# Performance work log

Hardware: AMD Instinct MI355X
Metric: run time of the kernel (lower is better)

Reference implementation:

```python
import jax, jax.numpy as jnp
import numpy as np

# Sampled 2-layer GraphSAGE sizes (ogbn-products-like, fanouts [25, 10], batch 4096)
N0, N1, N2 = 1_000_000, 40_960, 4_096   # source nodes per hop / targets
E1, E2 = 1_024_000, 40_960              # edges per hop
IN_C, HID, OUT = 100, 256, 47


def setup_inputs() -> dict:
    key = jax.random.key(0)
    ks = jax.random.split(key, 10)
    x = jax.random.normal(ks[0], (N0, IN_C), jnp.float32)
    src1 = jax.random.randint(ks[1], (E1,), 0, N0, dtype=jnp.int64)
    dst1 = jax.random.randint(ks[2], (E1,), 0, N1, dtype=jnp.int64)
    src2 = jax.random.randint(ks[3], (E2,), 0, N1, dtype=jnp.int64)
    dst2 = jax.random.randint(ks[4], (E2,), 0, N2, dtype=jnp.int64)
    s1 = 1.0 / np.sqrt(IN_C)
    s2 = 1.0 / np.sqrt(HID)
    W1l = jax.random.uniform(ks[5], (IN_C, HID), jnp.float32, -s1, s1)
    W1r = jax.random.uniform(ks[6], (IN_C, HID), jnp.float32, -s1, s1)
    b1l = jnp.zeros((HID,), jnp.float32)
    W2l = jax.random.uniform(ks[7], (HID, OUT), jnp.float32, -s2, s2)
    W2r = jax.random.uniform(ks[8], (HID, OUT), jnp.float32, -s2, s2)
    b2l = jnp.zeros((OUT,), jnp.float32)
    return {"x": x, "W1l": W1l, "b1l": b1l, "W1r": W1r,
            "W2l": W2l, "b2l": b2l, "W2r": W2r,
            "src1": src1, "dst1": dst1, "src2": src2, "dst2": dst2}


def _sage_conv(x_src, x_dst, src, dst, Wl, bl, Wr, num_dst):
    # PyG SAGEConv (aggr='mean'): lin_l(mean_j x_j) + lin_r(x_target)
    msg = x_src[src]                                            # [E, C] gather
    agg = jax.ops.segment_sum(msg, dst, num_segments=num_dst)   # [num_dst, C]
    cnt = jax.ops.segment_sum(jnp.ones((src.shape[0], 1), x_src.dtype), dst,
                              num_segments=num_dst)
    agg = agg / jnp.maximum(cnt, 1.0)                           # mean (0 for isolated)
    return agg @ Wl + bl + x_dst @ Wr


def reference(x, W1l, b1l, W1r, W2l, b2l, W2r, src1, dst1, src2, dst2):
    # layer 1: bipartite (N0 -> N1)
    h = _sage_conv(x, x[:N1], src1, dst1, W1l, b1l, W1r, N1)
    h = jax.nn.relu(h)  # dropout is identity in eval mode
    # layer 2: bipartite (N1 -> N2)
    out = _sage_conv(h, h[:N2], src2, dst2, W2l, b2l, W2r, N2)
    return jax.nn.log_softmax(out, axis=-1)
```

## Files before the change

kernel.cpp:

```cpp
#include <hip/hip_runtime.h>
#include <math.h>

#define N0 1000000
#define N1 40960
#define N2 4096
#define E1 1024000
#define E2 40960
#define IN_C 100
#define HID 256
#define OUT_C 47
#define S1 128
#define S2 64
#define KCAT 224
#define KSTEPS 7
#define LDSTR 232

typedef __attribute__((ext_vector_type(8))) short short8;
typedef __attribute__((ext_vector_type(4))) float float4v;

__device__ inline unsigned short f2bf(float f) {
    union { float f; unsigned u; } v; v.f = f;
    unsigned r = v.u + 0x7FFF + ((v.u >> 16) & 1);
    return (unsigned short)(r >> 16);
}

#define EDGE_BLKS ((E1 / 2 + E2 / 2) / 256)
#define PACK_BLKS 28
__global__ __launch_bounds__(256) void build_kernel(
    const int* __restrict__ src1, const int* __restrict__ dst1,
    const int* __restrict__ src2, const int* __restrict__ dst2,
    int* __restrict__ deg1, int* __restrict__ ell1,
    int* __restrict__ deg2, int* __restrict__ ell2,
    const float* __restrict__ W1l, const float* __restrict__ W1r,
    unsigned short* __restrict__ packedW) {
    if (blockIdx.x >= EDGE_BLKS) {
        int t = (blockIdx.x - EDGE_BLKS) * 256 + threadIdx.x;
        int nt = t / 448;
        int rem = t - nt * 448;
        int ks = rem >> 6;
        int lane = rem & 63;
        int n = nt * 16 + (lane & 15);
        int kbase = ks * 32 + (lane >> 4) * 8;
        unsigned short* wp = packedW + (size_t)(nt * 7 + ks) * 512 + lane * 8;
        #pragma unroll
        for (int j = 0; j < 8; ++j) {
            int k = kbase + j;
            float v = (k < 100) ? W1l[k * HID + n]
                    : (k < 200) ? W1r[(k - 100) * HID + n] : 0.f;
            wp[j] = f2bf(v);
        }
        return;
    }
    int gid = blockIdx.x * 256 + threadIdx.x;
    if (gid < E1 / 2) {
        int2 s = ((const int2*)src1)[gid];
        int2 d = ((const int2*)dst1)[gid];
        int slot0 = atomicAdd(&deg1[d.x], 1);
        if (slot0 < S1) ell1[d.x * S1 + slot0] = s.x;
        int slot1 = atomicAdd(&deg1[d.y], 1);
        if (slot1 < S1) ell1[d.y * S1 + slot1] = s.y;
    } else {
        int p = gid - E1 / 2;
        int2 s = ((const int2*)src2)[p];
        int2 d = ((const int2*)dst2)[p];
        int slot0 = atomicAdd(&deg2[d.x], 1);
        if (slot0 < S2) ell2[d.x * S2 + slot0] = s.x;
        int slot1 = atomicAdd(&deg2[d.y], 1);
        if (slot1 < S2) ell2[d.y * S2 + slot1] = s.y;
    }
}

__global__ __launch_bounds__(256) void agg_gemm1_kernel(
    const float* __restrict__ x, const int* __restrict__ ell1,
    const int* __restrict__ deg1,
    const unsigned short* __restrict__ packedW, const float* __restrict__ b1l,
    float* __restrict__ h) {
    __shared__ short As[32 * LDSTR];
    int tid = threadIdx.x;
    int i0 = blockIdx.x * 32;
    int lane = tid & 63;
    int w = tid >> 6;

    const float2* xs2 = (const float2*)(x + (size_t)i0 * IN_C);
    for (int idx = tid; idx < 32 * 50; idx += 256) {
        int r = idx / 50;
        int p = idx - r * 50;
        float2 v = xs2[idx];
        short2 o = {(short)f2bf(v.x), (short)f2bf(v.y)};
        *(short2*)(As + r * LDSTR + 100 + 2 * p) = o;
    }
    for (int idx = tid; idx < 32 * 12; idx += 256) {
        int r = idx / 12;
        int p = idx - r * 12;
        short2 z = {0, 0};
        *(short2*)(As + r * LDSTR + 200 + 2 * p) = z;
    }

    int l2 = (lane < 50) ? lane : 49;
    for (int rr = 0; rr < 8; ++rr) {
        int d = i0 + w * 8 + rr;
        int nd = deg1[d];
        int n = (nd < S1) ? nd : S1;
        const int* rp = ell1 + d * S1;

        float x0 = 0.f, y0 = 0.f, x1 = 0.f, y1 = 0.f;
        float x2 = 0.f, y2 = 0.f, x3 = 0.f, y3 = 0.f;
        int e = 0;
        for (; e + 7 < n; e += 8) {
            int s0 = rp[e],     s1 = rp[e + 1], s2 = rp[e + 2], s3 = rp[e + 3];
            int s4 = rp[e + 4], s5 = rp[e + 5], s6 = rp[e + 6], s7 = rp[e + 7];
            float2 v0 = ((const float2*)(x + s0 * IN_C))[l2];
            float2 v1 = ((const float2*)(x + s1 * IN_C))[l2];
            float2 v2 = ((const float2*)(x + s2 * IN_C))[l2];
            float2 v3 = ((const float2*)(x + s3 * IN_C))[l2];
            float2 v4 = ((const float2*)(x + s4 * IN_C))[l2];
            float2 v5 = ((const float2*)(x + s5 * IN_C))[l2];
            float2 v6 = ((const float2*)(x + s6 * IN_C))[l2];
            float2 v7 = ((const float2*)(x + s7 * IN_C))[l2];
            x0 += v0.x + v4.x; y0 += v0.y + v4.y;
            x1 += v1.x + v5.x; y1 += v1.y + v5.y;
            x2 += v2.x + v6.x; y2 += v2.y + v6.y;
            x3 += v3.x + v7.x; y3 += v3.y + v7.y;
        }
        for (; e + 1 < n; e += 2) {
            int s0 = rp[e], s1 = rp[e + 1];
            float2 v0 = ((const float2*)(x + s0 * IN_C))[l2];
            float2 v1 = ((const float2*)(x + s1 * IN_C))[l2];
            x0 += v0.x; y0 += v0.y;
            x1 += v1.x; y1 += v1.y;
        }
        if (e < n) {
            float2 v0 = ((const float2*)(x + rp[e] * IN_C))[l2];
            x0 += v0.x; y0 += v0.y;
        }
        float sx = (x0 + x1) + (x2 + x3);
        float sy = (y0 + y1) + (y2 + y3);
        float inv = 1.0f / (float)(nd > 0 ? nd : 1);
        if (lane < 50) {
            short2 o = {(short)f2bf(sx * inv), (short)f2bf(sy * inv)};
            *(short2*)(As + (w * 8 + rr) * LDSTR + 2 * lane) = o;
        }
    }
    __syncthreads();

    int quad = lane >> 4;
    int m = lane & 15;

    float4v acc[2][4];
    #pragma unroll
    for (int rt = 0; rt < 2; ++rt)
        #pragma unroll
        for (int c = 0; c < 4; ++c) acc[rt][c] = (float4v){0.f, 0.f, 0.f, 0.f};

    #pragma unroll
    for (int ks = 0; ks < KSTEPS; ++ks) {
        int ko = ks * 32 + quad * 8;
        short8 a0 = *(const short8*)(As + (0 * 16 + m) * LDSTR + ko);
        short8 a1 = *(const short8*)(As + (1 * 16 + m) * LDSTR + ko);
        #pragma unroll
        for (int c = 0; c < 4; ++c) {
            int nt = w * 4 + c;
            short8 b = *(const short8*)(packedW + (size_t)(nt * 7 + ks) * 512 + lane * 8);
            acc[0][c] = __builtin_amdgcn_mfma_f32_16x16x32_bf16(a0, b, acc[0][c], 0, 0, 0);
            acc[1][c] = __builtin_amdgcn_mfma_f32_16x16x32_bf16(a1, b, acc[1][c], 0, 0, 0);
        }
    }

    #pragma unroll
    for (int c = 0; c < 4; ++c) {
        int col = (w * 4 + c) * 16 + m;
        float bv = b1l[col];
        #pragma unroll
        for (int rt = 0; rt < 2; ++rt) {
            int rbase = i0 + rt * 16 + quad * 4;
            #pragma unroll
            for (int reg = 0; reg < 4; ++reg) {
                float v = acc[rt][c][reg] + bv;
                h[(size_t)(rbase + reg) * HID + col] = fmaxf(v, 0.f);
            }
        }
    }
}

__global__ __launch_bounds__(256) void l2_fused_kernel(
    const float* __restrict__ h, const int* __restrict__ ell2,
    const int* __restrict__ deg2,
    const float* __restrict__ W2l, const float* __restrict__ b2l,
    const float* __restrict__ W2r, float* __restrict__ out) {
    __shared__ float sa[4][HID];
    __shared__ float sh_[4][HID];
    int w = threadIdx.x >> 6;
    int lane = threadIdx.x & 63;
    int row = (blockIdx.x << 2) + w;

    int nd = deg2[row];
    int n = (nd < S2) ? nd : S2;
    const int* rp = ell2 + row * S2;
    float4 acc4 = {0.f, 0.f, 0.f, 0.f};
    int e = 0;
    for (; e + 1 < n; e += 2) {
        int s0 = rp[e], s1 = rp[e + 1];
        float4 v0 = ((const float4*)(h + s0 * HID))[lane];
        float4 v1 = ((const float4*)(h + s1 * HID))[lane];
        acc4.x += v0.x + v1.x; acc4.y += v0.y + v1.y;
        acc4.z += v0.z + v1.z; acc4.w += v0.w + v1.w;
    }
    if (e < n) {
        int s0 = rp[e];
        float4 v0 = ((const float4*)(h + s0 * HID))[lane];
        acc4.x += v0.x; acc4.y += v0.y; acc4.z += v0.z; acc4.w += v0.w;
    }
    float inv = 1.0f / (float)(nd > 0 ? nd : 1);
    float4 am = {acc4.x * inv, acc4.y * inv, acc4.z * inv, acc4.w * inv};
    ((float4*)&sa[w][0])[lane] = am;
    ((float4*)&sh_[w][0])[lane] = ((const float4*)(h + row * HID))[lane];
    __syncthreads();

    int j = lane;
    int jj = (j < OUT_C) ? j : (OUT_C - 1);
    float acc = 0.f;
    for (int k = 0; k < HID; k += 4) {
        float4 av = *(const float4*)&sa[w][k];
        float4 hv = *(const float4*)&sh_[w][k];
        acc += av.x * W2l[(k + 0) * OUT_C + jj] + hv.x * W2r[(k + 0) * OUT_C + jj];
        acc += av.y * W2l[(k + 1) * OUT_C + jj] + hv.y * W2r[(k + 1) * OUT_C + jj];
        acc += av.z * W2l[(k + 2) * OUT_C + jj] + hv.z * W2r[(k + 2) * OUT_C + jj];
        acc += av.w * W2l[(k + 3) * OUT_C + jj] + hv.w * W2r[(k + 3) * OUT_C + jj];
    }
    float v = acc + b2l[jj];
    float vm = (j < OUT_C) ? v : -__builtin_huge_valf();
    #pragma unroll
    for (int s = 32; s > 0; s >>= 1) vm = fmaxf(vm, __shfl_xor(vm, s));
    float ex = (j < OUT_C) ? __expf(v - vm) : 0.f;
    #pragma unroll
    for (int s = 32; s > 0; s >>= 1) ex += __shfl_xor(ex, s);
    if (j < OUT_C) out[row * OUT_C + j] = v - vm - __logf(ex);
}

extern "C" void kernel_launch(void* const* d_in, const int* in_sizes, int n_in,
                              void* d_out, int out_size, void* d_ws, size_t ws_size,
                              hipStream_t stream) {
    const float* x   = (const float*)d_in[0];
    const float* W1l = (const float*)d_in[1];
    const float* b1l = (const float*)d_in[2];
    const float* W1r = (const float*)d_in[3];
    const float* W2l = (const float*)d_in[4];
    const float* b2l = (const float*)d_in[5];
    const float* W2r = (const float*)d_in[6];
    const int* src1  = (const int*)d_in[7];
    const int* dst1  = (const int*)d_in[8];
    const int* src2  = (const int*)d_in[9];
    const int* dst2  = (const int*)d_in[10];
    float* out = (float*)d_out;

    char* ws = (char*)d_ws;
    size_t off = 0;
    auto alloc = [&](size_t bytes) {
        off = (off + 255) & ~(size_t)255;
        void* p = ws + off;
        off += bytes;
        return p;
    };

    int* deg1 = (int*)alloc(N1 * sizeof(int));
    int* deg2 = (int*)alloc(N2 * sizeof(int));
    int* ell1 = (int*)alloc((size_t)N1 * S1 * sizeof(int));
    int* ell2 = (int*)alloc((size_t)N2 * S2 * sizeof(int));
    float* h     = (float*)alloc((size_t)N1 * HID * sizeof(float));
    unsigned short* packedW = (unsigned short*)alloc((size_t)16 * 7 * 512 * sizeof(unsigned short));

    hipMemsetAsync(deg1, 0, (N1 + N2) * sizeof(int), stream);

    build_kernel<<<EDGE_BLKS + PACK_BLKS, 256, 0, stream>>>(
        src1, dst1, src2, dst2, deg1, ell1, deg2, ell2, W1l, W1r, packedW);
    agg_gemm1_kernel<<<N1 / 32, 256, 0, stream>>>(x, ell1, deg1, packedW, b1l, h);
    l2_fused_kernel<<<N2 / 4, 256, 0, stream>>>(h, ell2, deg2, W2l, b2l, W2r, out);
}
```

Measured before the change: 686.7 us.

## Merge three kernels into one cooperative persistent kernel with grid syncs

Replaces the build, layer-1 aggregate+GEMM and layer-2 fused kernels with a single cooperative kernel of 1024 blocks that uses grid.sync() between phases, looping over tiles persistently. This removes kernel launch gaps and tail effects between the three stages. The three-kernel path is kept as a fallback if the cooperative launch fails. The cost is that the grid is capped by co-residency, and layer 1 now gets fewer blocks than its 1280 tiles, which can reduce latency hiding on the memory-bound gather.

```diff
diff --git a/kernel.cpp b/kernel.cpp
--- a/kernel.cpp
+++ b/kernel.cpp
@@ -1,5 +1,8 @@
 #include <hip/hip_runtime.h>
+#include <hip/hip_cooperative_groups.h>
 #include <math.h>
+
+namespace cg = cooperative_groups;
 
 #define N0 1000000
 #define N1 40960
@@ -15,6 +18,9 @@
 #define KSTEPS 7
 #define LDSTR 232
 
+#define GRID_C 1024
+#define GSTRIDE (GRID_C * 256)
+
 typedef __attribute__((ext_vector_type(8))) short short8;
 typedef __attribute__((ext_vector_type(4))) float float4v;
 
@@ -22,6 +28,218 @@
     union { float f; unsigned u; } v; v.f = f;
     unsigned r = v.u + 0x7FFF + ((v.u >> 16) & 1);
     return (unsigned short)(r >> 16);
+}
+
+__global__ __launch_bounds__(256, 4) void mega_kernel(
+    const float* __restrict__ x,
+    const int* __restrict__ src1, const int* __restrict__ dst1,
+    const int* __restrict__ src2, const int* __restrict__ dst2,
+    int* __restrict__ deg1, int* __restrict__ ell1,
+    int* __restrict__ deg2, int* __restrict__ ell2,
+    const float* __restrict__ W1l, const float* __restrict__ W1r,
+    const float* __restrict__ b1l,
+    const float* __restrict__ W2l, const float* __restrict__ b2l,
+    const float* __restrict__ W2r,
+    unsigned short* __restrict__ packedW,
+    float* __restrict__ h, float* __restrict__ out) {
+    __shared__ short As[32 * LDSTR];
+    __shared__ float sa[4][HID];
+    __shared__ float sh_[4][HID];
+
+    cg::grid_group grid = cg::this_grid();
+    int tid = threadIdx.x;
+    int bid = blockIdx.x;
+    int gtid = bid * 256 + tid;
+    int lane = tid & 63;
+    int w = tid >> 6;
+
+    if (gtid < 7168) {
+        int nt = gtid / 448;
+        int rem = gtid - nt * 448;
+        int ks = rem >> 6;
+        int pl = rem & 63;
+        int n = nt * 16 + (pl & 15);
+        int kbase = ks * 32 + (pl >> 4) * 8;
+        unsigned short* wp = packedW + (size_t)(nt * 7 + ks) * 512 + pl * 8;
+        #pragma unroll
+        for (int j = 0; j < 8; ++j) {
+            int k = kbase + j;
+            float v = (k < 100) ? W1l[k * HID + n]
+                    : (k < 200) ? W1r[(k - 100) * HID + n] : 0.f;
+            wp[j] = f2bf(v);
+        }
+    }
+    for (int u = gtid; u < E1 / 2 + E2 / 2; u += GSTRIDE) {
+        if (u < E1 / 2) {
+            int2 s = ((const int2*)src1)[u];
+            int2 d = ((const int2*)dst1)[u];
+            int slot0 = atomicAdd(&deg1[d.x], 1);
+            if (slot0 < S1) ell1[d.x * S1 + slot0] = s.x;
+            int slot1 = atomicAdd(&deg1[d.y], 1);
+            if (slot1 < S1) ell1[d.y * S1 + slot1] = s.y;
+        } else {
+            int p = u - E1 / 2;
+            int2 s = ((const int2*)src2)[p];
+            int2 d = ((const int2*)dst2)[p];
+            int slot0 = atomicAdd(&deg2[d.x], 1);
+            if (slot0 < S2) ell2[d.x * S2 + slot0] = s.x;
+            int slot1 = atomicAdd(&deg2[d.y], 1);
+            if (slot1 < S2) ell2[d.y * S2 + slot1] = s.y;
+        }
+    }
+    grid.sync();
+
+    for (int t = bid; t < N1 / 32; t += GRID_C) {
+        int i0 = t * 32;
+
+        const float2* xs2 = (const float2*)(x + (size_t)i0 * IN_C);
+        for (int idx = tid; idx < 32 * 50; idx += 256) {
+            int r = idx / 50;
+            int p = idx - r * 50;
+            float2 v = xs2[idx];
+            short2 o = {(short)f2bf(v.x), (short)f2bf(v.y)};
+            *(short2*)(As + r * LDSTR + 100 + 2 * p) = o;
+        }
+        for (int idx = tid; idx < 32 * 12; idx += 256) {
+            int r = idx / 12;
+            int p = idx - r * 12;
+            short2 z = {0, 0};
+            *(short2*)(As + r * LDSTR + 200 + 2 * p) = z;
+        }
+
+        int l2 = (lane < 50) ? lane : 49;
+        for (int rr = 0; rr < 8; ++rr) {
+            int d = i0 + w * 8 + rr;
+            int nd = deg1[d];
+            int n = (nd < S1) ? nd : S1;
+            const int* rp = ell1 + d * S1;
+
+            float x0 = 0.f, y0 = 0.f, x1 = 0.f, y1 = 0.f;
+            float x2 = 0.f, y2 = 0.f, x3 = 0.f, y3 = 0.f;
+            int e = 0;
+            for (; e + 7 < n; e += 8) {
+                int s0 = rp[e],     s1 = rp[e + 1], s2 = rp[e + 2], s3 = rp[e + 3];
+                int s4 = rp[e + 4], s5 = rp[e + 5], s6 = rp[e + 6], s7 = rp[e + 7];
+                float2 v0 = ((const float2*)(x + s0 * IN_C))[l2];
+                float2 v1 = ((const float2*)(x + s1 * IN_C))[l2];
+                float2 v2 = ((const float2*)(x + s2 * IN_C))[l2];
+                float2 v3 = ((const float2*)(x + s3 * IN_C))[l2];
+                float2 v4 = ((const float2*)(x + s4 * IN_C))[l2];
+                float2 v5 = ((const float2*)(x + s5 * IN_C))[l2];
+                float2 v6 = ((const float2*)(x + s6 * IN_C))[l2];
+                float2 v7 = ((const float2*)(x + s7 * IN_C))[l2];
+                x0 += v0.x + v4.x; y0 += v0.y + v4.y;
+                x1 += v1.x + v5.x; y1 += v1.y + v5.y;
+                x2 += v2.x + v6.x; y2 += v2.y + v6.y;
+                x3 += v3.x + v7.x; y3 += v3.y + v7.y;
+            }
+            for (; e + 1 < n; e += 2) {
+                int s0 = rp[e], s1 = rp[e + 1];
+                float2 v0 = ((const float2*)(x + s0 * IN_C))[l2];
+                float2 v1 = ((const float2*)(x + s1 * IN_C))[l2];
+                x0 += v0.x; y0 += v0.y;
+                x1 += v1.x; y1 += v1.y;
+            }
+            if (e < n) {
+                float2 v0 = ((const float2*)(x + rp[e] * IN_C))[l2];
+                x0 += v0.x; y0 += v0.y;
+            }
+            float sx = (x0 + x1) + (x2 + x3);
+            float sy = (y0 + y1) + (y2 + y3);
+            float inv = 1.0f / (float)(nd > 0 ? nd : 1);
+            if (lane < 50) {
+                short2 o = {(short)f2bf(sx * inv), (short)f2bf(sy * inv)};
+                *(short2*)(As + (w * 8 + rr) * LDSTR + 2 * lane) = o;
+            }
+        }
+        __syncthreads();
+
+        int quad = lane >> 4;
+        int m = lane & 15;
+
+        float4v acc[2][4];
+        #pragma unroll
+        for (int rt = 0; rt < 2; ++rt)
+            #pragma unroll
+            for (int c = 0; c < 4; ++c) acc[rt][c] = (float4v){0.f, 0.f, 0.f, 0.f};
+
+        #pragma unroll
+        for (int ks = 0; ks < KSTEPS; ++ks) {
+            int ko = ks * 32 + quad * 8;
+            short8 a0 = *(const short8*)(As + (0 * 16 + m) * LDSTR + ko);
+            short8 a1 = *(const short8*)(As + (1 * 16 + m) * LDSTR + ko);
+            #pragma unroll
+            for (int c = 0; c < 4; ++c) {
+                int nt = w * 4 + c;
+                short8 b = *(const short8*)(packedW + (size_t)(nt * 7 + ks) * 512 + lane * 8);
+                acc[0][c] = __builtin_amdgcn_mfma_f32_16x16x32_bf16(a0, b, acc[0][c], 0, 0, 0);
+                acc[1][c] = __builtin_amdgcn_mfma_f32_16x16x32_bf16(a1, b, acc[1][c], 0, 0, 0);
+            }
+        }
+
+        #pragma unroll
+        for (int c = 0; c < 4; ++c) {
+            int col = (w * 4 + c) * 16 + m;
+            float bv = b1l[col];
+            #pragma unroll
+            for (int rt = 0; rt < 2; ++rt) {
+                int rbase = i0 + rt * 16 + quad * 4;
+                #pragma unroll
+                for (int reg = 0; reg < 4; ++reg) {
+                    float v = acc[rt][c][reg] + bv;
+                    h[(size_t)(rbase + reg) * HID + col] = fmaxf(v, 0.f);
+                }
+            }
+        }
+        __syncthreads();
+    }
+    grid.sync();
+
+    {
+        int row = (bid << 2) + w;
+        int nd = deg2[row];
+        int n = (nd < S2) ? nd : S2;
+        const int* rp = ell2 + row * S2;
+        float4 acc4 = {0.f, 0.f, 0.f, 0.f};
+        int e = 0;
+        for (; e + 1 < n; e += 2) {
+            int s0 = rp[e], s1 = rp[e + 1];
+            float4 v0 = ((const float4*)(h + s0 * HID))[lane];
+            float4 v1 = ((const float4*)(h + s1 * HID))[lane];
+            acc4.x += v0.x + v1.x; acc4.y += v0.y + v1.y;
+            acc4.z += v0.z + v1.z; acc4.w += v0.w + v1.w;
+        }
+        if (e < n) {
+            int s0 = rp[e];
+            float4 v0 = ((const float4*)(h + s0 * HID))[lane];
+            acc4.x += v0.x; acc4.y += v0.y; acc4.z += v0.z; acc4.w += v0.w;
+        }
+        float inv = 1.0f / (float)(nd > 0 ? nd : 1);
+        float4 am = {acc4.x * inv, acc4.y * inv, acc4.z * inv, acc4.w * inv};
+        ((float4*)&sa[w][0])[lane] = am;
+        ((float4*)&sh_[w][0])[lane] = ((const float4*)(h + row * HID))[lane];
+        __syncthreads();
+
+        int j = lane;
+        int jj = (j < OUT_C) ? j : (OUT_C - 1);
+        float acc = 0.f;
+        for (int k = 0; k < HID; k += 4) {
+            float4 av = *(const float4*)&sa[w][k];
+            float4 hv = *(const float4*)&sh_[w][k];
+            acc += av.x * W2l[(k + 0) * OUT_C + jj] + hv.x * W2r[(k + 0) * OUT_C + jj];
+            acc += av.y * W2l[(k + 1) * OUT_C + jj] + hv.y * W2r[(k + 1) * OUT_C + jj];
+            acc += av.z * W2l[(k + 2) * OUT_C + jj] + hv.z * W2r[(k + 2) * OUT_C + jj];
+            acc += av.w * W2l[(k + 3) * OUT_C + jj] + hv.w * W2r[(k + 3) * OUT_C + jj];
+        }
+        float v = acc + b2l[jj];
+        float vm = (j < OUT_C) ? v : -__builtin_huge_valf();
+        #pragma unroll
+        for (int s = 32; s > 0; s >>= 1) vm = fmaxf(vm, __shfl_xor(vm, s));
+        float ex = (j < OUT_C) ? __expf(v - vm) : 0.f;
+        #pragma unroll
+        for (int s = 32; s > 0; s >>= 1) ex += __shfl_xor(ex, s);
+        if (j < OUT_C) out[row * OUT_C + j] = v - vm - __logf(ex);
+    }
 }
 
 #define EDGE_BLKS ((E1 / 2 + E2 / 2) / 256)
@@ -271,8 +489,18 @@
 
     hipMemsetAsync(deg1, 0, (N1 + N2) * sizeof(int), stream);
 
-    build_kernel<<<EDGE_BLKS + PACK_BLKS, 256, 0, stream>>>(
-        src1, dst1, src2, dst2, deg1, ell1, deg2, ell2, W1l, W1r, packedW);
-    agg_gemm1_kernel<<<N1 / 32, 256, 0, stream>>>(x, ell1, deg1, packedW, b1l, h);
-    l2_fused_kernel<<<N2 / 4, 256, 0, stream>>>(h, ell2, deg2, W2l, b2l, W2r, out);
+    void* args[] = {
+        (void*)&x, (void*)&src1, (void*)&dst1, (void*)&src2, (void*)&dst2,
+        (void*)&deg1, (void*)&ell1, (void*)&deg2, (void*)&ell2,
+        (void*)&W1l, (void*)&W1r, (void*)&b1l,
+        (void*)&W2l, (void*)&b2l, (void*)&W2r,
+        (void*)&packedW, (void*)&h, (void*)&out};
+    hipError_t err = hipLaunchCooperativeKernel(
+        (const void*)mega_kernel, dim3(GRID_C), dim3(256), args, 0, stream);
+    if (err != hipSuccess) {
+        build_kernel<<<EDGE_BLKS + PACK_BLKS, 256, 0, stream>>>(
+            src1, dst1, src2, dst2, deg1, ell1, deg2, ell2, W1l, W1r, packedW);
+        agg_gemm1_kernel<<<N1 / 32, 256, 0, stream>>>(x, ell1, deg1, packedW, b1l, h);
+        l2_fused_kernel<<<N2 / 4, 256, 0, stream>>>(h, ell2, deg2, W2l, b2l, W2r, out);
+    }
 }
```

New measurement: 936.1 us. 1.36x slower.
